# Kernel tuning notes

Measured on AMD Instinct MI355X. Metric: run time of the kernel, lower is better.

## Reference

```python
import jax, jax.numpy as jnp
import numpy as np

B, HID, R, K, NC = 8192, 512, 16, 512, 16


def setup_inputs() -> dict:
    key = jax.random.key(0)
    k1, k2, k3, k4 = jax.random.split(key, 4)
    x = jax.random.normal(k1, (B, 1, K, R), dtype=jnp.float32)
    W = jax.random.normal(k2, (HID, R, K), dtype=jnp.float32) * (1.0 / np.sqrt(K))
    V = jax.random.normal(k3, (NC, HID), dtype=jnp.float32) * (1.0 / np.sqrt(HID))
    b = jax.random.normal(k4, (NC,), dtype=jnp.float32)
    return {"x": x, "W": W, "V": V, "b": b}


def reference(x, W, V, b):
    # Original: full batched matmul(W, x) -> [B, HID, R, R], then diagonal over
    # (dim2, dim3) and sum over R. Mathematically identical to computing only
    # the diagonal entries and summing: s[b,h] = sum_r sum_k W[h,r,k] * x[b,0,k,r].
    s = jnp.einsum('hrk,bkr->bh', W, x[:, 0])  # [B, HID]
    h = jnp.tanh(s)
    return h @ V.T + b  # [B, NC]
```

## Files before the change

### kernel.cpp

```cpp
#include <hip/hip_runtime.h>
#include <hip/hip_bf16.h>
#include <math.h>

typedef float f32x4 __attribute__((ext_vector_type(4)));
typedef __bf16 bf16x8 __attribute__((ext_vector_type(8)));

constexpr int B   = 8192;
constexpr int HID = 512;
constexpr int R   = 16;
constexpr int K   = 512;
constexpr int NC  = 16;
constexpr int KK  = R * K;
constexpr int BM  = 128, BN = 128, BK = 64;
constexpr int NT  = KK / BK;

__device__ inline unsigned pack_bf16(float a, float b) {
  unsigned ua = __builtin_bit_cast(unsigned, a) + 0x8000u;
  unsigned ub = __builtin_bit_cast(unsigned, b) + 0x8000u;
  return __builtin_amdgcn_perm(ub, ua, 0x07060302u);
}

__device__ inline int swz(int row, int colbyte) {
  return row * 128 + (colbyte ^ ((row & 7) << 4));
}

__global__ void wconv_kernel(const float* __restrict__ W, ushort* __restrict__ Wt) {
  int t = blockIdx.x * blockDim.x + threadIdx.x;
  int h = t >> 9, k = t & (K - 1);
  const float* src = W + (size_t)h * KK + k;
  unsigned pk[8];
#pragma unroll
  for (int rp = 0; rp < 8; ++rp) {
    float a = src[(size_t)(2 * rp) * K];
    float b = src[(size_t)(2 * rp + 1) * K];
    pk[rp] = pack_bf16(a, b);
  }
  uint4* dst = reinterpret_cast<uint4*>(Wt + (size_t)h * KK + k * R);
  dst[0] = make_uint4(pk[0], pk[1], pk[2], pk[3]);
  dst[1] = make_uint4(pk[4], pk[5], pk[6], pk[7]);
}

__global__ __launch_bounds__(512, 1)
void gemm_tanh_kernel(const float* __restrict__ x, const ushort* __restrict__ Wt,
                      float* __restrict__ hout) {
  __shared__ ushort ldsA[2][BM * BK];
  __shared__ ushort ldsB[2][BN * BK];

  int bid = blockIdx.x;
  int xcd = bid & 7, j = bid >> 3;
  int mt = xcd * 8 + (j >> 2), ntile = j & 3;
  int m_base = mt * BM, n_base = ntile * BN;

  int t = threadIdx.x;
  int lane = t & 63, wid = t >> 6;
  int wm = wid >> 2, wn = wid & 3;

  const float*  xg = x  + (size_t)m_base * KK;
  const ushort* wg = Wt + (size_t)n_base * KK;

  f32x4 areg[4];
  uint4 breg[2];

  auto loadTile = [&](int kt) {
    int koff = kt * BK;
#pragma unroll
    for (int p = 0; p < 4; ++p) {
      int g = t + p * 512;
      int row = g >> 4, col = (g & 15) * 4;
      areg[p] = *reinterpret_cast<const f32x4*>(xg + (size_t)row * KK + koff + col);
    }
#pragma unroll
    for (int p = 0; p < 2; ++p) {
      int g = t + p * 512;
      int row = g >> 3, col = (g & 7) * 8;
      breg[p] = *reinterpret_cast<const uint4*>(wg + (size_t)row * KK + koff + col);
    }
  };

  auto writeTile = [&](int buf) {
    char* baseA = reinterpret_cast<char*>(ldsA[buf]);
    char* baseB = reinterpret_cast<char*>(ldsB[buf]);
#pragma unroll
    for (int p = 0; p < 4; ++p) {
      int g = t + p * 512;
      int row = g >> 4, colb = (g & 15) * 8;
      unsigned lo = pack_bf16(areg[p].x, areg[p].y);
      unsigned hi = pack_bf16(areg[p].z, areg[p].w);
      *reinterpret_cast<uint2*>(baseA + swz(row, colb)) = make_uint2(lo, hi);
    }
#pragma unroll
    for (int p = 0; p < 2; ++p) {
      int g = t + p * 512;
      int row = g >> 3, colb = (g & 7) * 16;
      *reinterpret_cast<uint4*>(baseB + swz(row, colb)) = breg[p];
    }
  };

  f32x4 acc[4][2] = {};

  loadTile(0);
  writeTile(0);
  __syncthreads();
  loadTile(1);

  int cur = 0;
  for (int tt = 0; tt < NT; ++tt) {
    if (tt + 1 < NT) {
      writeTile(cur ^ 1);
      if (tt + 2 < NT) loadTile(tt + 2);
    }
    const char* baseA = reinterpret_cast<const char*>(ldsA[cur]);
    const char* baseB = reinterpret_cast<const char*>(ldsB[cur]);
#pragma unroll
    for (int kk = 0; kk < 2; ++kk) {
      int kb = kk * 64 + (lane >> 4) * 16;
      bf16x8 af[4], bfr[2];
#pragma unroll
      for (int m = 0; m < 4; ++m) {
        int row = wm * 64 + m * 16 + (lane & 15);
        af[m] = *reinterpret_cast<const bf16x8*>(baseA + swz(row, kb));
      }
#pragma unroll
      for (int n = 0; n < 2; ++n) {
        int row = wn * 32 + n * 16 + (lane & 15);
        bfr[n] = *reinterpret_cast<const bf16x8*>(baseB + swz(row, kb));
      }
#pragma unroll
      for (int m = 0; m < 4; ++m)
#pragma unroll
        for (int n = 0; n < 2; ++n)
          acc[m][n] = __builtin_amdgcn_mfma_f32_16x16x32_bf16(af[m], bfr[n], acc[m][n], 0, 0, 0);
    }
    __syncthreads();
    cur ^= 1;
  }

#pragma unroll
  for (int m = 0; m < 4; ++m) {
    int row0 = m_base + wm * 64 + m * 16 + (lane >> 4) * 4;
#pragma unroll
    for (int n = 0; n < 2; ++n) {
      int col = n_base + wn * 32 + n * 16 + (lane & 15);
#pragma unroll
      for (int jj = 0; jj < 4; ++jj)
        hout[(size_t)(row0 + jj) * HID + col] = tanhf(acc[m][n][jj]);
    }
  }
}

__global__ __launch_bounds__(256)
void proj_kernel(const float* __restrict__ hbuf, const float* __restrict__ V,
                 const float* __restrict__ bias, float* __restrict__ out) {
  __shared__ float Vs[NC * HID];
  int t = threadIdx.x;
#pragma unroll
  for (int p = 0; p < 8; ++p) {
    int g = t + p * 256;
    reinterpret_cast<f32x4*>(Vs)[g] = reinterpret_cast<const f32x4*>(V)[g];
  }
  __syncthreads();
  int wid = t >> 6, lane = t & 63;
  int brow = blockIdx.x * 4 + wid;
  const float* hr = hbuf + (size_t)brow * HID;
  float hv[8];
#pragma unroll
  for (int jj = 0; jj < 8; ++jj) hv[jj] = hr[jj * 64 + lane];
  float acc[NC];
#pragma unroll
  for (int c = 0; c < NC; ++c) acc[c] = 0.f;
#pragma unroll
  for (int jj = 0; jj < 8; ++jj)
#pragma unroll
    for (int c = 0; c < NC; ++c)
      acc[c] += hv[jj] * Vs[c * HID + jj * 64 + lane];
  float myval = 0.f;
#pragma unroll
  for (int c = 0; c < NC; ++c) {
    float s = acc[c];
#pragma unroll
    for (int off = 32; off > 0; off >>= 1) s += __shfl_xor(s, off);
    if (lane == c) myval = s;
  }
  if (lane < NC) out[(size_t)brow * NC + lane] = myval + bias[lane];
}

extern "C" void kernel_launch(void* const* d_in, const int* in_sizes, int n_in,
                              void* d_out, int out_size, void* d_ws, size_t ws_size,
                              hipStream_t stream) {
  const float* x = (const float*)d_in[0];
  const float* W = (const float*)d_in[1];
  const float* V = (const float*)d_in[2];
  const float* b = (const float*)d_in[3];
  float* out = (float*)d_out;

  ushort* Wt   = (ushort*)d_ws;
  float*  hbuf = (float*)((char*)d_ws + (size_t)HID * KK * sizeof(ushort));

  wconv_kernel<<<HID * K / 256, 256, 0, stream>>>(W, Wt);
  gemm_tanh_kernel<<<(B / BM) * (HID / BN), 512, 0, stream>>>(x, Wt, hbuf);
  proj_kernel<<<B / 4, 256, 0, stream>>>(hbuf, V, b, out);
}
```

Baseline: 520.2 us.

## Split GEMM K dimension in two and load W tiles directly into LDS

The GEMM's K dimension is split into two halves, doubling the grid from 256 to 512 blocks. Each half writes fp32 partial sums, and the projection kernel adds the two partials and applies a fast exp-based tanh. B tiles now go from global memory straight into LDS via global_load_lds with the swizzle applied on the source address, skipping the register staging. Launch bounds allow more blocks per CU. The cost is an extra partial buffer write and read of about 16 MB each way.

```diff
diff --git a/kernel.cpp b/kernel.cpp
--- a/kernel.cpp
+++ b/kernel.cpp
@@ -4,6 +4,9 @@
 
 typedef float f32x4 __attribute__((ext_vector_type(4)));
 typedef __bf16 bf16x8 __attribute__((ext_vector_type(8)));
+
+#define GLOBAL_AS __attribute__((address_space(1)))
+#define LDS_AS    __attribute__((address_space(3)))
 
 constexpr int B   = 8192;
 constexpr int HID = 512;
@@ -12,7 +15,9 @@
 constexpr int NC  = 16;
 constexpr int KK  = R * K;
 constexpr int BM  = 128, BN = 128, BK = 64;
-constexpr int NT  = KK / BK;
+constexpr int KSPLIT = 2;
+constexpr int KS  = KK / KSPLIT;
+constexpr int NTK = KS / BK;
 
 __device__ inline unsigned pack_bf16(float a, float b) {
   unsigned ua = __builtin_bit_cast(unsigned, a) + 0x8000u;
@@ -40,46 +45,40 @@
   dst[1] = make_uint4(pk[4], pk[5], pk[6], pk[7]);
 }
 
-__global__ __launch_bounds__(512, 1)
-void gemm_tanh_kernel(const float* __restrict__ x, const ushort* __restrict__ Wt,
-                      float* __restrict__ hout) {
+__global__ __launch_bounds__(512, 4)
+void gemm_splitk_kernel(const float* __restrict__ x, const ushort* __restrict__ Wt,
+                        float* __restrict__ part) {
   __shared__ ushort ldsA[2][BM * BK];
   __shared__ ushort ldsB[2][BN * BK];
 
   int bid = blockIdx.x;
   int xcd = bid & 7, j = bid >> 3;
-  int mt = xcd * 8 + (j >> 2), ntile = j & 3;
-  int m_base = mt * BM, n_base = ntile * BN;
+  int mt = xcd * 8 + (j >> 3);
+  int kc = (j >> 2) & 1, nt = j & 3;
+  int m_base = mt * BM, n_base = nt * BN;
 
   int t = threadIdx.x;
   int lane = t & 63, wid = t >> 6;
   int wm = wid >> 2, wn = wid & 3;
 
-  const float*  xg = x  + (size_t)m_base * KK;
-  const ushort* wg = Wt + (size_t)n_base * KK;
+  const float* xg = x + (size_t)m_base * KK + (size_t)kc * KS;
+  const char*  bg = (const char*)(Wt + (size_t)n_base * KK + (size_t)kc * KS);
+  float* pout = part + (size_t)kc * B * HID;
 
   f32x4 areg[4];
-  uint4 breg[2];
-
-  auto loadTile = [&](int kt) {
-    int koff = kt * BK;
+
+  auto loadA = [&](int tt) {
+    int koff = tt * BK;
 #pragma unroll
     for (int p = 0; p < 4; ++p) {
       int g = t + p * 512;
       int row = g >> 4, col = (g & 15) * 4;
       areg[p] = *reinterpret_cast<const f32x4*>(xg + (size_t)row * KK + koff + col);
     }
-#pragma unroll
-    for (int p = 0; p < 2; ++p) {
-      int g = t + p * 512;
-      int row = g >> 3, col = (g & 7) * 8;
-      breg[p] = *reinterpret_cast<const uint4*>(wg + (size_t)row * KK + koff + col);
-    }
   };
 
-  auto writeTile = [&](int buf) {
+  auto writeA = [&](int buf) {
     char* baseA = reinterpret_cast<char*>(ldsA[buf]);
-    char* baseB = reinterpret_cast<char*>(ldsB[buf]);
 #pragma unroll
     for (int p = 0; p < 4; ++p) {
       int g = t + p * 512;
@@ -88,26 +87,37 @@
       unsigned hi = pack_bf16(areg[p].z, areg[p].w);
       *reinterpret_cast<uint2*>(baseA + swz(row, colb)) = make_uint2(lo, hi);
     }
+  };
+
+  auto gldB = [&](int buf, int tt) {
+    char* lb = reinterpret_cast<char*>(ldsB[buf]);
 #pragma unroll
     for (int p = 0; p < 2; ++p) {
-      int g = t + p * 512;
-      int row = g >> 3, colb = (g & 7) * 16;
-      *reinterpret_cast<uint4*>(baseB + swz(row, colb)) = breg[p];
+      int chunk = p * 8 + wid;
+      int o = chunk * 1024 + lane * 16;
+      int r = o >> 7, cb = o & 127;
+      size_t soff = (size_t)r * (KK * 2) + (size_t)(cb ^ ((r & 7) << 4)) + (size_t)tt * 128;
+      __builtin_amdgcn_global_load_lds(
+          (const GLOBAL_AS void*)(bg + soff),
+          (LDS_AS void*)(lb + chunk * 1024),
+          16, 0, 0);
     }
   };
 
   f32x4 acc[4][2] = {};
 
-  loadTile(0);
-  writeTile(0);
+  loadA(0);
+  gldB(0, 0);
+  writeA(0);
   __syncthreads();
-  loadTile(1);
+  loadA(1);
 
   int cur = 0;
-  for (int tt = 0; tt < NT; ++tt) {
-    if (tt + 1 < NT) {
-      writeTile(cur ^ 1);
-      if (tt + 2 < NT) loadTile(tt + 2);
+  for (int tt = 0; tt < NTK; ++tt) {
+    if (tt + 1 < NTK) {
+      gldB(cur ^ 1, tt + 1);
+      writeA(cur ^ 1);
+      if (tt + 2 < NTK) loadA(tt + 2);
     }
     const char* baseA = reinterpret_cast<const char*>(ldsA[cur]);
     const char* baseB = reinterpret_cast<const char*>(ldsB[cur]);
@@ -143,14 +153,21 @@
       int col = n_base + wn * 32 + n * 16 + (lane & 15);
 #pragma unroll
       for (int jj = 0; jj < 4; ++jj)
-        hout[(size_t)(row0 + jj) * HID + col] = tanhf(acc[m][n][jj]);
-    }
-  }
+        pout[(size_t)(row0 + jj) * HID + col] = acc[m][n][jj];
+    }
+  }
+}
+
+__device__ inline float tanh_fast(float s) {
+  float e = __expf(-2.f * fabsf(s));
+  float t = (1.f - e) / (1.f + e);
+  return copysignf(t, s);
 }
 
 __global__ __launch_bounds__(256)
-void proj_kernel(const float* __restrict__ hbuf, const float* __restrict__ V,
-                 const float* __restrict__ bias, float* __restrict__ out) {
+void proj_kernel(const float* __restrict__ p0, const float* __restrict__ p1,
+                 const float* __restrict__ V, const float* __restrict__ bias,
+                 float* __restrict__ out) {
   __shared__ float Vs[NC * HID];
   int t = threadIdx.x;
 #pragma unroll
@@ -161,10 +178,14 @@
   __syncthreads();
   int wid = t >> 6, lane = t & 63;
   int brow = blockIdx.x * 4 + wid;
-  const float* hr = hbuf + (size_t)brow * HID;
+  const float* r0 = p0 + (size_t)brow * HID;
+  const float* r1 = p1 + (size_t)brow * HID;
   float hv[8];
 #pragma unroll
-  for (int jj = 0; jj < 8; ++jj) hv[jj] = hr[jj * 64 + lane];
+  for (int jj = 0; jj < 8; ++jj) {
+    float s = r0[jj * 64 + lane] + r1[jj * 64 + lane];
+    hv[jj] = tanh_fast(s);
+  }
   float acc[NC];
 #pragma unroll
   for (int c = 0; c < NC; ++c) acc[c] = 0.f;
@@ -194,9 +215,11 @@
   float* out = (float*)d_out;
 
   ushort* Wt   = (ushort*)d_ws;
-  float*  hbuf = (float*)((char*)d_ws + (size_t)HID * KK * sizeof(ushort));
+  float*  part = (float*)((char*)d_ws + (size_t)HID * KK * 2);
+  float*  p0 = part;
+  float*  p1 = part + (size_t)B * HID;
 
   wconv_kernel<<<HID * K / 256, 256, 0, stream>>>(W, Wt);
-  gemm_tanh_kernel<<<(B / BM) * (HID / BN), 512, 0, stream>>>(x, Wt, hbuf);
-  proj_kernel<<<B / 4, 256, 0, stream>>>(hbuf, V, b, out);
-}
+  gemm_splitk_kernel<<<(B / BM) * (HID / BN) * KSPLIT, 512, 0, stream>>>(x, Wt, part);
+  proj_kernel<<<B / 4, 256, 0, stream>>>(p0, p1, V, b, out);
+}
```

Result: faster. 450.4 us (-13.4%).
